# Kernel tuning notes

Hardware: AMD Instinct MI355X
Metric: run time of the kernel (lower is better)

Reference implementation:

```python
import jax, jax.numpy as jnp
import numpy as np

B, T, F, H = 64, 512, 512, 1024

def setup_inputs() -> dict:
    key = jax.random.key(0)
    k1, k2, k3, k4 = jax.random.split(key, 4)
    std = 1.0 / np.sqrt(H)
    return {
        "x": jax.random.normal(k1, (B, T, F), dtype=jnp.float32),
        "U": jax.random.normal(k2, (F, 4 * H), dtype=jnp.float32) * (1.0 / np.sqrt(F)),
        "W": jax.random.normal(k3, (H, 4 * H), dtype=jnp.float32) * std,
        "b": jax.random.uniform(k4, (4 * H,), dtype=jnp.float32, minval=-std, maxval=std),
    }

def reference(x, U, W, b):
    Bsz, Tlen, _ = x.shape
    Hs = W.shape[0]
    # Precompute input projection for all timesteps: [T, B, 4H]
    xU = jnp.einsum('btf,fg->tbg', x, U) + b
    h0 = jnp.zeros((Bsz, Hs), dtype=x.dtype)
    c0 = jnp.zeros((Bsz, Hs), dtype=x.dtype)

    def step(carry, xu_t):
        h_t, c_t = carry
        gates = xu_t + h_t @ W  # [B, 4H]
        f_t = jax.nn.sigmoid(gates[:, :Hs])
        i_t = jax.nn.sigmoid(gates[:, Hs:2 * Hs])
        o_t = jax.nn.sigmoid(gates[:, 2 * Hs:3 * Hs])
        c_tilde = jax.nn.sigmoid(gates[:, 3 * Hs:])  # faithful: original uses sigmoid here
        c_t = f_t * c_t + i_t * c_tilde
        h_t = o_t * jnp.tanh(c_t)
        return (h_t, c_t), h_t

    (h_T, c_T), hs = jax.lax.scan(step, (h0, c0), xU)
    hidden_seq = jnp.transpose(hs, (1, 0, 2))  # [B, T, H]
    return hidden_seq, h_T, c_T
```

## Files before the change

kernel.cpp:

```cpp
#include <hip/hip_runtime.h>


#define Bz 64
#define Tz 512
#define Fz 512
#define Hz 1024
#define ROWP16 1544
#define ROWP64 386
#define NBLK 256
#define NTHR 512

typedef unsigned short u16;
typedef unsigned int u32;
typedef unsigned long long u64;
typedef __attribute__((ext_vector_type(8))) short bf16x8;
typedef __attribute__((ext_vector_type(4))) float f32x4;

__device__ __forceinline__ u16 f2bf(float f) {
    union { float f; unsigned u; } v; v.f = f;
    unsigned r = v.u + 0x7FFFu + ((v.u >> 16) & 1u);
    return (u16)(r >> 16);
}
__device__ __forceinline__ float fast_sigmoid(float x) {
    return 1.0f / (1.0f + __expf(-x));
}
__device__ __forceinline__ float fast_tanh(float x) {
    float e = __expf(2.0f * x);
    return 1.0f - 2.0f / (e + 1.0f);
}

__global__ __launch_bounds__(256) void conv_x_kernel(const float* __restrict__ x,
                                                     u16* __restrict__ xb) {
    size_t i = (size_t)blockIdx.x * 256 + threadIdx.x;
    float4 v = ((const float4*)x)[i];
    ushort4 o;
    o.x = f2bf(v.x); o.y = f2bf(v.y); o.z = f2bf(v.z); o.w = f2bf(v.w);
    ((ushort4*)xb)[i] = o;
}

__global__ __launch_bounds__(256) void transpose_tile_kernel(const float* __restrict__ src,
                                                             u16* __restrict__ dst,
                                                             int K, int N) {
    __shared__ u16 tile[32][33];
    const int ntk = K >> 5;
    const int tk = blockIdx.x % ntk;
    const int tn = blockIdx.x / ntk;
    const int c = threadIdx.x & 31;
    const int r0 = threadIdx.x >> 5;
#pragma unroll
    for (int rr = 0; rr < 32; rr += 8) {
        const int r = r0 + rr;
        tile[r][c] = f2bf(src[(size_t)(tk * 32 + r) * N + tn * 32 + c]);
    }
    __syncthreads();
#pragma unroll
    for (int rr = 0; rr < 32; rr += 8) {
        const int r = r0 + rr;
        dst[(size_t)(tn * 32 + r) * K + tk * 32 + c] = tile[c][r];
    }
}

__global__ __launch_bounds__(256) void init_state_kernel(u32* __restrict__ h0,
                                                         u32* __restrict__ flags) {
    int i = blockIdx.x * 256 + threadIdx.x;
    h0[i] = 0u;
    if (i < 256) flags[i] = 0u;
}

__global__ __launch_bounds__(NTHR, 1) void lstm_persist(
    const u16* __restrict__ xb,
    const u16* __restrict__ UT,
    const u16* __restrict__ WT,
    const float* __restrict__ bias,
    u64* __restrict__ h0,
    u64* __restrict__ h1,
    float* __restrict__ out,
    u32* __restrict__ flags) {

    __shared__ __align__(16) u16 albuf[16 * ROWP16];
    __shared__ float gbuf[2][4 * 16 * 17];

    const int tid = threadIdx.x;
    const int w = tid >> 6;
    const int g = w & 3;
    const int kh = w >> 2;
    const int l = tid & 63;
    const int lr = l & 15;
    const int lk = l >> 4;
    const int bg = blockIdx.x >> 6;
    const int jg = blockIdx.x & 63;
    const int mbase = bg * 16;
    const int jbase = jg * 16;
    const int n = g * Hz + jbase + lr;

    bf16x8 bwU[8], bwW[16];
    {
        const u16* Ub = UT + (size_t)n * Fz + kh * 256 + lk * 8;
        const u16* Wb = WT + (size_t)n * Hz + kh * 512 + lk * 8;
#pragma unroll
        for (int kb = 0; kb < 8; ++kb)  bwU[kb] = *(const bf16x8*)(Ub + kb * 32);
#pragma unroll
        for (int kb = 0; kb < 16; ++kb) bwW[kb] = *(const bf16x8*)(Wb + kb * 32);
    }

    const int ml_e = (tid & 255) >> 4;
    const int jj_e = tid & 15;
    const int m_e = mbase + ml_e;
    const int j_e = jbase + jj_e;
    float creg = 0.0f;
    float bv4[4];
#pragma unroll
    for (int gg = 0; gg < 4; ++gg) bv4[gg] = bias[gg * Hz + jbase + jj_e];

    const size_t OFF_HT = (size_t)Bz * Tz * Hz;
    const size_t OFF_CT = OFF_HT + (size_t)Bz * Hz;

    const u32* __restrict__ flg = flags + bg * 64;
    u64* albuf64 = (u64*)albuf;

    bf16x8 tx[2], txn[2];
#pragma unroll
    for (int it = 0; it < 2; ++it) {
        int idx = it * NTHR + tid;
        int ml = idx >> 6, ci = idx & 63;
        tx[it] = *(const bf16x8*)(xb + ((size_t)(mbase + ml) * Tz + 0) * Fz + ci * 8);
    }

#pragma unroll 1
    for (int t = 0; t < Tz; ++t) {
        const u64* __restrict__ hin  = (t & 1) ? h1 : h0;
        u64* __restrict__ hout       = (t & 1) ? h0 : h1;

#pragma unroll
        for (int it = 0; it < 2; ++it) {
            int idx = it * NTHR + tid;
            int ml = idx >> 6, ci = idx & 63;
            *(bf16x8*)(albuf + ml * ROWP16 + ci * 8) = tx[it];
        }
        __syncthreads();

        if (t + 1 < Tz) {
#pragma unroll
            for (int it = 0; it < 2; ++it) {
                int idx = it * NTHR + tid;
                int ml = idx >> 6, ci = idx & 63;
                txn[it] = *(const bf16x8*)(xb + ((size_t)(mbase + ml) * Tz + (t + 1)) * Fz + ci * 8);
            }
        }

        u32 pv = 0;
        if (t) pv = __hip_atomic_load(flg + l, __ATOMIC_RELAXED,
                                      __HIP_MEMORY_SCOPE_AGENT);

        f32x4 a0 = {0.f,0.f,0.f,0.f}, a1 = a0, a2 = a0, a3 = a0;
        {
            const u16* abase = albuf + lr * ROWP16 + kh * 256 + lk * 8;
#pragma unroll
            for (int kb = 0; kb < 8; kb += 4) {
                a0 = __builtin_amdgcn_mfma_f32_16x16x32_bf16(*(const bf16x8*)(abase + (kb+0)*32), bwU[kb+0], a0, 0,0,0);
                a1 = __builtin_amdgcn_mfma_f32_16x16x32_bf16(*(const bf16x8*)(abase + (kb+1)*32), bwU[kb+1], a1, 0,0,0);
                a2 = __builtin_amdgcn_mfma_f32_16x16x32_bf16(*(const bf16x8*)(abase + (kb+2)*32), bwU[kb+2], a2, 0,0,0);
                a3 = __builtin_amdgcn_mfma_f32_16x16x32_bf16(*(const bf16x8*)(abase + (kb+3)*32), bwU[kb+3], a3, 0,0,0);
            }
        }

        if (t) {
            const unsigned tgt = (unsigned)t;
            u32 v = pv;
            while (!__all((int)(v >= tgt)))
                v = __hip_atomic_load(flg + l, __ATOMIC_RELAXED,
                                      __HIP_MEMORY_SCOPE_AGENT);
        }

        {
            u64 hv[8];
            const u64* hsrc = hin + (size_t)mbase * 256;
#pragma unroll
            for (int r = 0; r < 8; ++r)
                hv[r] = __hip_atomic_load(hsrc + r * NTHR + tid, __ATOMIC_RELAXED,
                                          __HIP_MEMORY_SCOPE_AGENT);
#pragma unroll
            for (int r = 0; r < 8; ++r) {
                int idx = r * NTHR + tid;
                int ml = idx >> 8, ci = idx & 255;
                albuf64[ml * ROWP64 + 128 + ci] = hv[r];
            }
        }
        __syncthreads();

        {
            const u16* abase = albuf + lr * ROWP16 + 512 + kh * 512 + lk * 8;
#pragma unroll
            for (int kb = 0; kb < 16; kb += 4) {
                a0 = __builtin_amdgcn_mfma_f32_16x16x32_bf16(*(const bf16x8*)(abase + (kb+0)*32), bwW[kb+0], a0, 0,0,0);
                a1 = __builtin_amdgcn_mfma_f32_16x16x32_bf16(*(const bf16x8*)(abase + (kb+1)*32), bwW[kb+1], a1, 0,0,0);
                a2 = __builtin_amdgcn_mfma_f32_16x16x32_bf16(*(const bf16x8*)(abase + (kb+2)*32), bwW[kb+2], a2, 0,0,0);
                a3 = __builtin_amdgcn_mfma_f32_16x16x32_bf16(*(const bf16x8*)(abase + (kb+3)*32), bwW[kb+3], a3, 0,0,0);
            }
        }
        f32x4 acc = (a0 + a1) + (a2 + a3);

#pragma unroll
        for (int i = 0; i < 4; ++i)
            gbuf[kh][g * 272 + (lk * 4 + i) * 17 + lr] = acc[i];
        __syncthreads();

        float hn = 0.0f, cn = 0.0f;
        if (tid < 256) {
            const int q = ml_e * 17 + jj_e;
            float fg = fast_sigmoid(gbuf[0][q]        + gbuf[1][q]        + bv4[0]);
            float ig = fast_sigmoid(gbuf[0][272 + q]  + gbuf[1][272 + q]  + bv4[1]);
            float og = fast_sigmoid(gbuf[0][544 + q]  + gbuf[1][544 + q]  + bv4[2]);
            float ct = fast_sigmoid(gbuf[0][816 + q]  + gbuf[1][816 + q]  + bv4[3]);
            cn = fg * creg + ig * ct;
            creg = cn;
            hn = og * fast_tanh(cn);
            float hn1 = __shfl_xor(hn, 1);
            u32 p01 = ((u32)f2bf(hn1) << 16) | (u32)f2bf(hn);
            u32 p23 = __shfl_xor(p01, 2);
            if (!(jj_e & 3)) {
                u64 pk = ((u64)p23 << 32) | (u64)p01;
                __hip_atomic_store(hout + (size_t)m_e * 256 + (j_e >> 2), pk,
                                   __ATOMIC_RELAXED, __HIP_MEMORY_SCOPE_AGENT);
            }
        }

        if (t != Tz - 1) {
            __syncthreads();
            if (tid == 0)
                __hip_atomic_store((u32*)flg + jg, (u32)(t + 1),
                                   __ATOMIC_RELAXED, __HIP_MEMORY_SCOPE_AGENT);
        }

        if (tid < 256) {
            out[((size_t)m_e * Tz + t) * Hz + j_e] = hn;
            if (t == Tz - 1) {
                out[OFF_HT + (size_t)m_e * Hz + j_e] = hn;
                out[OFF_CT + (size_t)m_e * Hz + j_e] = cn;
            }
        }
        tx[0] = txn[0];
        tx[1] = txn[1];
    }
}

extern "C" void kernel_launch(void* const* d_in, const int* in_sizes, int n_in,
                              void* d_out, int out_size, void* d_ws, size_t ws_size,
                              hipStream_t stream) {
    const float* x    = (const float*)d_in[0];
    const float* U    = (const float*)d_in[1];
    const float* W    = (const float*)d_in[2];
    const float* bias = (const float*)d_in[3];
    float* out = (float*)d_out;
    char* ws = (char*)d_ws;

    u16* xb    = (u16*)(ws + 0);
    u16* UT    = (u16*)(ws + 33554432);
    u16* WT    = (u16*)(ws + 37748736);
    u64* h0    = (u64*)(ws + 46137344);
    u64* h1    = (u64*)(ws + 46268416);
    u32* flags = (u32*)(ws + 46399488);

    conv_x_kernel<<<16384, 256, 0, stream>>>(x, xb);
    transpose_tile_kernel<<<2048, 256, 0, stream>>>(U, UT, 512, 4096);
    transpose_tile_kernel<<<4096, 256, 0, stream>>>(W, WT, 1024, 4096);
    init_state_kernel<<<128, 256, 0, stream>>>((u32*)h0, flags);

    lstm_persist<<<NBLK, NTHR, 0, stream>>>(xb, UT, WT, bias, h0, h1, out, flags);
}
```

Before: 1.462 ms.

## Block the h exchange layout and defer hidden-sequence output to an unpack kernel

The recurrent h buffer is reordered so each block's 16x16 tile of packed bf16 h values is contiguous, for both the per-step store and the neighbour loads. Inside the persistent loop, the fp32 hidden-sequence writes (strided across many rows) are replaced by contiguous stores of packed bf16 values into a workspace scratch buffer. A separate kernel then expands that buffer into the fp32 output. This takes scattered global writes off the latency-critical recurrence, at the cost of an extra kernel pass over memory and bf16-rounded hidden-sequence outputs. The scratch path only runs if the workspace is large enough.

Result: slower. 1.524 ms (+4.2%).

```diff
diff --git a/kernel.cpp b/kernel.cpp
--- a/kernel.cpp
+++ b/kernel.cpp
@@ -67,6 +67,23 @@
     if (i < 256) flags[i] = 0u;
 }
 
+__global__ __launch_bounds__(256) void unpack_out_kernel(const u64* __restrict__ oscr,
+                                                         float* __restrict__ out) {
+    const unsigned g = blockIdx.x * 256 + threadIdx.x;
+    const int jq = g & 255;
+    const int t = (g >> 8) & 511;
+    const int b = g >> 17;
+    const int bg = b >> 4, ml = b & 15;
+    const int jg = jq >> 2, q = jq & 3;
+    u64 pk = oscr[(size_t)t * 16384 + bg * 4096 + jg * 64 + ml * 4 + q];
+    float4 v;
+    v.x = __uint_as_float((u32)(pk & 0xFFFFu) << 16);
+    v.y = __uint_as_float((u32)((pk >> 16) & 0xFFFFu) << 16);
+    v.z = __uint_as_float((u32)((pk >> 32) & 0xFFFFu) << 16);
+    v.w = __uint_as_float((u32)(pk >> 48) << 16);
+    *(float4*)(out + ((size_t)b * Tz + t) * Hz + jq * 4) = v;
+}
+
 __global__ __launch_bounds__(NTHR, 1) void lstm_persist(
     const u16* __restrict__ xb,
     const u16* __restrict__ UT,
@@ -75,7 +92,8 @@
     u64* __restrict__ h0,
     u64* __restrict__ h1,
     float* __restrict__ out,
-    u32* __restrict__ flags) {
+    u32* __restrict__ flags,
+    u64* __restrict__ oscr) {
 
     __shared__ __align__(16) u16 albuf[16 * ROWP16];
     __shared__ float gbuf[2][4 * 16 * 17];
@@ -117,6 +135,7 @@
 
     const u32* __restrict__ flg = flags + bg * 64;
     u64* albuf64 = (u64*)albuf;
+    const int hblk = bg * 4096 + jg * 64;
 
     bf16x8 tx[2], txn[2];
 #pragma unroll
@@ -174,16 +193,16 @@
 
         {
             u64 hv[8];
-            const u64* hsrc = hin + (size_t)mbase * 256;
+            const u64* hsrc = hin + bg * 4096;
 #pragma unroll
             for (int r = 0; r < 8; ++r)
                 hv[r] = __hip_atomic_load(hsrc + r * NTHR + tid, __ATOMIC_RELAXED,
                                           __HIP_MEMORY_SCOPE_AGENT);
 #pragma unroll
             for (int r = 0; r < 8; ++r) {
-                int idx = r * NTHR + tid;
-                int ml = idx >> 8, ci = idx & 255;
-                albuf64[ml * ROWP64 + 128 + ci] = hv[r];
+                int e = r * NTHR + tid;
+                int ml = (e >> 2) & 15, jgs = e >> 6, q = e & 3;
+                albuf64[ml * ROWP64 + 128 + (jgs << 2) + q] = hv[r];
             }
         }
         __syncthreads();
@@ -205,6 +224,7 @@
             gbuf[kh][g * 272 + (lk * 4 + i) * 17 + lr] = acc[i];
         __syncthreads();
 
+        u64 pk = 0;
         float hn = 0.0f, cn = 0.0f;
         if (tid < 256) {
             const int q = ml_e * 17 + jj_e;
@@ -219,8 +239,8 @@
             u32 p01 = ((u32)f2bf(hn1) << 16) | (u32)f2bf(hn);
             u32 p23 = __shfl_xor(p01, 2);
             if (!(jj_e & 3)) {
-                u64 pk = ((u64)p23 << 32) | (u64)p01;
-                __hip_atomic_store(hout + (size_t)m_e * 256 + (j_e >> 2), pk,
+                pk = ((u64)p23 << 32) | (u64)p01;
+                __hip_atomic_store(hout + hblk + ml_e * 4 + (jj_e >> 2), pk,
                                    __ATOMIC_RELAXED, __HIP_MEMORY_SCOPE_AGENT);
             }
         }
@@ -233,12 +253,18 @@
         }
 
         if (tid < 256) {
-            out[((size_t)m_e * Tz + t) * Hz + j_e] = hn;
+            if (oscr) {
+                if (!(jj_e & 3))
+                    oscr[(size_t)t * 16384 + hblk + ml_e * 4 + (jj_e >> 2)] = pk;
+            } else {
+                out[((size_t)m_e * Tz + t) * Hz + j_e] = hn;
+            }
             if (t == Tz - 1) {
                 out[OFF_HT + (size_t)m_e * Hz + j_e] = hn;
                 out[OFF_CT + (size_t)m_e * Hz + j_e] = cn;
             }
         }
+
         tx[0] = txn[0];
         tx[1] = txn[1];
     }
@@ -260,11 +286,16 @@
     u64* h0    = (u64*)(ws + 46137344);
     u64* h1    = (u64*)(ws + 46268416);
     u32* flags = (u32*)(ws + 46399488);
+    const size_t OSCR_OFF = 46400512;
+    const size_t OSCR_BYTES = (size_t)Tz * 16384 * 8;
+    u64* oscr = (ws_size >= OSCR_OFF + OSCR_BYTES) ? (u64*)(ws + OSCR_OFF) : (u64*)0;
 
     conv_x_kernel<<<16384, 256, 0, stream>>>(x, xb);
     transpose_tile_kernel<<<2048, 256, 0, stream>>>(U, UT, 512, 4096);
     transpose_tile_kernel<<<4096, 256, 0, stream>>>(W, WT, 1024, 4096);
     init_state_kernel<<<128, 256, 0, stream>>>((u32*)h0, flags);
 
-    lstm_persist<<<NBLK, NTHR, 0, stream>>>(xb, UT, WT, bias, h0, h1, out, flags);
-}
+    lstm_persist<<<NBLK, NTHR, 0, stream>>>(xb, UT, WT, bias, h0, h1, out, flags, oscr);
+    if (oscr)
+        unpack_out_kernel<<<32768, 256, 0, stream>>>(oscr, out);
+}
```
